# Optimization experiments

Hardware: AMD Instinct MI355X
Metric: run time of the kernel (lower is better)

## Reference

```python
import jax, jax.numpy as jnp
import numpy as np
from jax import lax


def setup_inputs() -> dict:
    key = jax.random.key(0)
    k1, k2 = jax.random.split(key)
    B, L1, L2, D = 128, 512, 512, 16
    s1_batch = jax.random.normal(k1, (B, L1, D), dtype=jnp.float32)
    s2_batch = jax.random.normal(k2, (B, L2, D), dtype=jnp.float32)
    return {"s1_batch": s1_batch, "s2_batch": s2_batch}


def _pairwise_sq_dists(s1, s2):
    # C[b,i,j] = sum_d (s1[b,i,d] - s2[b,j,d])^2, computed without a [B,L1,L2,D] temp
    s1sq = jnp.sum(s1 * s1, axis=-1)  # [B, L1]
    s2sq = jnp.sum(s2 * s2, axis=-1)  # [B, L2]
    cross = jnp.einsum("bid,bjd->bij", s1, s2)  # [B, L1, L2]
    return s1sq[:, :, None] + s2sq[:, None, :] - 2.0 * cross


def _dtw_final(C):
    # C: [B, L1, L2] cost matrix; returns DTW[:, -1, -1] via row-wise scan
    # Row 0: DTW[0, j] = cumsum of costs (only left moves allowed)
    row0 = jnp.cumsum(C[:, 0, :], axis=1)  # [B, L2]

    def row_step(prev_row, c_row):
        # prev_row, c_row: [B, L2]
        first = c_row[:, 0] + prev_row[:, 0]  # j = 0: only 'up' predecessor
        cs = c_row[:, 1:].T      # [L2-1, B]
        ups = prev_row[:, 1:].T  # DTW[i-1, j]
        dgs = prev_row[:, :-1].T # DTW[i-1, j-1]

        def col_step(left, xs):
            c_j, up, dg = xs
            val = c_j + jnp.minimum(left, jnp.minimum(up, dg))
            return val, val

        _, rest = lax.scan(col_step, first, (cs, ups, dgs))  # rest: [L2-1, B]
        new_row = jnp.concatenate([first[:, None], rest.T], axis=1)
        return new_row, None

    final_row, _ = lax.scan(row_step, row0, jnp.moveaxis(C[:, 1:, :], 1, 0))
    return final_row[:, -1]  # [B]


def reference(s1_batch, s2_batch):
    C = _pairwise_sq_dists(s1_batch, s2_batch)
    dtw_end = _dtw_final(C)
    return jnp.mean(jnp.sqrt(dtw_end))
```

## Files before the change

kernel.cpp:

```cpp
#include <hip/hip_runtime.h>
#include <math.h>


#define TL 512
#define TD 16
#define TNB 128
#define BIGF 3.0e38f
#define INFF __builtin_inff()
#define WOFF 71
#define EP 8
#define NE 99

typedef float f32x2 __attribute__((ext_vector_type(2)));
typedef float f32x4 __attribute__((ext_vector_type(4)));

__device__ inline f32x2 pk_fma(f32x2 a, f32x2 b, f32x2 c) {
    f32x2 d;
    asm("v_pk_fma_f32 %0, %1, %2, %3" : "=v"(d) : "v"(a), "v"(b), "v"(c));
    return d;
}
__device__ inline f32x2 pk_mul(f32x2 a, f32x2 b) {
    f32x2 d;
    asm("v_pk_mul_f32 %0, %1, %2" : "=v"(d) : "v"(a), "v"(b));
    return d;
}
__device__ inline float min3f(float a, float b, float c) {
    float d;
    asm("v_min3_f32 %0, %1, %2, %3" : "=v"(d) : "v"(a), "v"(b), "v"(c));
    return d;
}
template<int CTRL, int RM, bool BC>
__device__ inline float dpp_mov(float old_, float src) {
    return __int_as_float(__builtin_amdgcn_update_dpp(
        __float_as_int(old_), __float_as_int(src), CTRL, RM, 0xf, BC));
}

struct XR { f32x4 q0, q1, q2, q3; float sq; };

__device__ inline void xissue(unsigned xb, unsigned sb, int r, XR& x) {
    int rc = r < 0 ? 0 : (r > TL - 1 ? TL - 1 : r);
    unsigned a16 = xb + ((unsigned)rc << 4);
    unsigned a4  = sb + ((unsigned)rc << 2);
    asm volatile("ds_read_b128 %0, %1 offset:0"     : "=v"(x.q0) : "v"(a16));
    asm volatile("ds_read_b128 %0, %1 offset:8192"  : "=v"(x.q1) : "v"(a16));
    asm volatile("ds_read_b128 %0, %1 offset:16384" : "=v"(x.q2) : "v"(a16));
    asm volatile("ds_read_b128 %0, %1 offset:24576" : "=v"(x.q3) : "v"(a16));
    asm volatile("ds_read_b32  %0, %1 offset:0"     : "=v"(x.sq) : "v"(a4));
}

#define WAITC() { asm volatile("s_waitcnt lgkmcnt(10)" ::: "memory"); \
                  __builtin_amdgcn_sched_barrier(0); }

__device__ inline void sub(const XR& x, int r,
                           const f32x2 (&y0)[8], const f32x2 (&y1)[8],
                           f32x2 ys0, f32x2 ys1,
                           float& pv0, float& pv1, float& o1,
                           float bL, float bD, bool lane0) {
    const f32x2* xd = (const f32x2*)&x;
    f32x2 a0 = ys0, a1 = ys1;
    #pragma unroll
    for (int k = 0; k < 8; ++k) {
        a0 = pk_fma(xd[k], y0[k], a0);
        a1 = pk_fma(xd[k], y1[k], a1);
    }
    const float c0 = x.sq + (a0.x + a0.y);
    const float c1 = x.sq + (a1.x + a1.y);

    float left = dpp_mov<0x138, 0xf, false>(BIGF, pv1);
    float diag = dpp_mov<0x138, 0xf, false>(BIGF, o1);
    if (lane0) { left = bL; diag = bD; }
    o1 = pv1;

    const float v0 = c0 + min3f(pv0, left, diag);
    const float v1 = c1 + min3f(pv1, v0, pv0);
    const bool valid = (unsigned)r < (unsigned)TL;
    pv0 = valid ? v0 : pv0;
    pv1 = valid ? v1 : pv1;
}

__global__ __launch_bounds__(256, 1) void dtw_split_kernel(const float* __restrict__ s1,
                                                           const float* __restrict__ s2,
                                                           float* __restrict__ ws) {
    const int b   = blockIdx.x;
    const int tid = threadIdx.x;
    const int W   = tid >> 6;
    const int l   = tid & 63;

    __shared__ f32x4 xT[4][TL];
    __shared__ float sqT[TL];
    __shared__ f32x4 pkt[2][4][2];

    const float* s1b = s1 + (size_t)b * TL * TD;

    #pragma unroll
    for (int q = 0; q < 2; ++q) {
        const int r = 2 * tid + q;
        const f32x4* src = (const f32x4*)(s1b + r * TD);
        f32x4 q0 = src[0], q1 = src[1], q2 = src[2], q3 = src[3];
        xT[0][r] = q0; xT[1][r] = q1; xT[2][r] = q2; xT[3][r] = q3;
        f32x2 a_ = pk_mul(f32x2{q0.x, q0.y}, f32x2{q0.x, q0.y});
        a_ = pk_fma(f32x2{q0.z, q0.w}, f32x2{q0.z, q0.w}, a_);
        a_ = pk_fma(f32x2{q1.x, q1.y}, f32x2{q1.x, q1.y}, a_);
        a_ = pk_fma(f32x2{q1.z, q1.w}, f32x2{q1.z, q1.w}, a_);
        a_ = pk_fma(f32x2{q2.x, q2.y}, f32x2{q2.x, q2.y}, a_);
        a_ = pk_fma(f32x2{q2.z, q2.w}, f32x2{q2.z, q2.w}, a_);
        a_ = pk_fma(f32x2{q3.x, q3.y}, f32x2{q3.x, q3.y}, a_);
        a_ = pk_fma(f32x2{q3.z, q3.w}, f32x2{q3.z, q3.w}, a_);
        sqT[r] = a_.x + a_.y;
    }
    if (tid < 64) ((float*)pkt)[tid] = BIGF;

    const int j0 = 2 * (64 * W + l);
    f32x2 y0[8], y1[8];
    const float* yp0 = s2 + ((size_t)b * TL + j0) * TD;
    #pragma unroll
    for (int k = 0; k < 8; ++k) {
        y0[k] = *(const f32x2*)(yp0 + 2 * k);
        y1[k] = *(const f32x2*)(yp0 + TD + 2 * k);
    }
    f32x2 s0a = pk_mul(y0[0], y0[0]), s1a = pk_mul(y1[0], y1[0]);
    #pragma unroll
    for (int k = 1; k < 8; ++k) {
        s0a = pk_fma(y0[k], y0[k], s0a);
        s1a = pk_fma(y1[k], y1[k], s1a);
    }
    const f32x2 ys0 = {s0a.x + s0a.y, 0.f};
    const f32x2 ys1 = {s1a.x + s1a.y, 0.f};
    #pragma unroll
    for (int k = 0; k < 8; ++k) {
        y0[k] = pk_mul(y0[k], f32x2{-2.f, -2.f});
        y1[k] = pk_mul(y1[k], f32x2{-2.f, -2.f});
    }

    __syncthreads();

    const unsigned xb = (unsigned)(uintptr_t)&xT[0][0];
    const unsigned sb = (unsigned)(uintptr_t)&sqT[0];
    const int gL = WOFF * W + l;
    const bool lane0 = (l == 0);
    float pv0 = INFF, pv1 = INFF, o1 = INFF;
    float carry = (W == 0) ? 0.f : BIGF;

    XR x0, x1, x2, x3;
    xissue(xb, sb, 0 - gL, x0);
    xissue(xb, sb, 1 - gL, x1);
    xissue(xb, sb, 2 - gL, x2);

    for (int e = 0; e < NE; ++e) {
        float lb0 = BIGF, lb1 = BIGF, lb2 = BIGF, lb3 = BIGF;
        float lb4 = BIGF, lb5 = BIGF, lb6 = BIGF, lb7 = BIGF;
        if (W > 0) {
            f32x4 pA = pkt[(e + 1) & 1][W - 1][0];
            f32x4 pB = pkt[(e + 1) & 1][W - 1][1];
            lb0 = pA.x; lb1 = pA.y; lb2 = pA.z; lb3 = pA.w;
            lb4 = pB.x; lb5 = pB.y; lb6 = pB.z; lb7 = pB.w;
        }
        const int rb = EP * e - gL;
        float t0, t1, t2, t3, t4, t5, t6, t7;

        WAITC(); xissue(xb, sb, rb + 3,  x3);
        sub(x0, rb + 0, y0, y1, ys0, ys1, pv0, pv1, o1, lb0, carry, lane0); t0 = pv1;
        WAITC(); xissue(xb, sb, rb + 4,  x0);
        sub(x1, rb + 1, y0, y1, ys0, ys1, pv0, pv1, o1, lb1, lb0, lane0);   t1 = pv1;
        WAITC(); xissue(xb, sb, rb + 5,  x1);
        sub(x2, rb + 2, y0, y1, ys0, ys1, pv0, pv1, o1, lb2, lb1, lane0);   t2 = pv1;
        WAITC(); xissue(xb, sb, rb + 6,  x2);
        sub(x3, rb + 3, y0, y1, ys0, ys1, pv0, pv1, o1, lb3, lb2, lane0);   t3 = pv1;
        WAITC(); xissue(xb, sb, rb + 7,  x3);
        sub(x0, rb + 4, y0, y1, ys0, ys1, pv0, pv1, o1, lb4, lb3, lane0);   t4 = pv1;
        WAITC(); xissue(xb, sb, rb + 8,  x0);
        sub(x1, rb + 5, y0, y1, ys0, ys1, pv0, pv1, o1, lb5, lb4, lane0);   t5 = pv1;
        WAITC(); xissue(xb, sb, rb + 9,  x1);
        sub(x2, rb + 6, y0, y1, ys0, ys1, pv0, pv1, o1, lb6, lb5, lane0);   t6 = pv1;
        WAITC(); xissue(xb, sb, rb + 10, x2);
        sub(x3, rb + 7, y0, y1, ys0, ys1, pv0, pv1, o1, lb7, lb6, lane0);   t7 = pv1;

        carry = lb7;

        if (l == 63 && W < 3) {
            pkt[e & 1][W][0] = f32x4{t0, t1, t2, t3};
            pkt[e & 1][W][1] = f32x4{t4, t5, t6, t7};
        }
        __syncthreads();
    }

    if (W == 3 && l == 63) ws[b] = sqrtf(pv1);
}

__global__ void dtw_reduce_kernel(const float* __restrict__ ws, float* __restrict__ out) {
    const int t = threadIdx.x;
    float v = ws[t] + ws[t + 64];
    #pragma unroll
    for (int d2 = 32; d2 > 0; d2 >>= 1) v += __shfl_down(v, d2);
    if (t == 0) out[0] = v * (1.0f / TNB);
}

extern "C" void kernel_launch(void* const* d_in, const int* in_sizes, int n_in,
                              void* d_out, int out_size, void* d_ws, size_t ws_size,
                              hipStream_t stream) {
    const float* s1 = (const float*)d_in[0];
    const float* s2 = (const float*)d_in[1];
    float* ws  = (float*)d_ws;
    float* out = (float*)d_out;

    dtw_split_kernel<<<TNB, 256, 0, stream>>>(s1, s2, ws);
    dtw_reduce_kernel<<<1, 64, 0, stream>>>(ws, out);
}
```

Before: 95.95 us.

## Assign four DTW columns per thread and run the wavefront with two waves

Each thread now owns four adjacent columns of the DTW matrix instead of two, so a block uses two wavefronts (128 threads) instead of four. The anti-diagonal pipeline shortens from 99 to 81 epochs, and fewer inter-wave handoffs and barriers are needed. In exchange, each step does twice the packed-FMA work and has a longer serial min-add chain per thread. Only half as many SIMDs per CU are used.

```diff
diff --git a/kernel.cpp b/kernel.cpp
--- a/kernel.cpp
+++ b/kernel.cpp
@@ -9,7 +9,7 @@
 #define INFF __builtin_inff()
 #define WOFF 71
 #define EP 8
-#define NE 99
+#define NE 81
 
 typedef float f32x2 __attribute__((ext_vector_type(2)));
 typedef float f32x4 __attribute__((ext_vector_type(4)));
@@ -53,32 +53,41 @@
 
 __device__ inline void sub(const XR& x, int r,
                            const f32x2 (&y0)[8], const f32x2 (&y1)[8],
-                           f32x2 ys0, f32x2 ys1,
-                           float& pv0, float& pv1, float& o1,
-                           float bL, float bD, bool lane0) {
+                           const f32x2 (&y2)[8], const f32x2 (&y3)[8],
+                           f32x2 ys0, f32x2 ys1, f32x2 ys2, f32x2 ys3,
+                           float& pv0, float& pv1, float& pv2, float& pv3,
+                           float& o3, float bL, float bD, bool lane0) {
     const f32x2* xd = (const f32x2*)&x;
-    f32x2 a0 = ys0, a1 = ys1;
+    f32x2 a0 = ys0, a1 = ys1, a2 = ys2, a3 = ys3;
     #pragma unroll
     for (int k = 0; k < 8; ++k) {
         a0 = pk_fma(xd[k], y0[k], a0);
         a1 = pk_fma(xd[k], y1[k], a1);
+        a2 = pk_fma(xd[k], y2[k], a2);
+        a3 = pk_fma(xd[k], y3[k], a3);
     }
     const float c0 = x.sq + (a0.x + a0.y);
     const float c1 = x.sq + (a1.x + a1.y);
-
-    float left = dpp_mov<0x138, 0xf, false>(BIGF, pv1);
-    float diag = dpp_mov<0x138, 0xf, false>(BIGF, o1);
+    const float c2 = x.sq + (a2.x + a2.y);
+    const float c3 = x.sq + (a3.x + a3.y);
+
+    float left = dpp_mov<0x138, 0xf, false>(BIGF, pv3);
+    float diag = dpp_mov<0x138, 0xf, false>(BIGF, o3);
     if (lane0) { left = bL; diag = bD; }
-    o1 = pv1;
+    o3 = pv3;
 
     const float v0 = c0 + min3f(pv0, left, diag);
     const float v1 = c1 + min3f(pv1, v0, pv0);
+    const float v2 = c2 + min3f(pv2, v1, pv1);
+    const float v3 = c3 + min3f(pv3, v2, pv2);
     const bool valid = (unsigned)r < (unsigned)TL;
     pv0 = valid ? v0 : pv0;
     pv1 = valid ? v1 : pv1;
-}
-
-__global__ __launch_bounds__(256, 1) void dtw_split_kernel(const float* __restrict__ s1,
+    pv2 = valid ? v2 : pv2;
+    pv3 = valid ? v3 : pv3;
+}
+
+__global__ __launch_bounds__(128, 1) void dtw_split_kernel(const float* __restrict__ s1,
                                                            const float* __restrict__ s2,
                                                            float* __restrict__ ws) {
     const int b   = blockIdx.x;
@@ -88,13 +97,13 @@
 
     __shared__ f32x4 xT[4][TL];
     __shared__ float sqT[TL];
-    __shared__ f32x4 pkt[2][4][2];
+    __shared__ f32x4 pkt[2][2];
 
     const float* s1b = s1 + (size_t)b * TL * TD;
 
     #pragma unroll
-    for (int q = 0; q < 2; ++q) {
-        const int r = 2 * tid + q;
+    for (int q = 0; q < 4; ++q) {
+        const int r = tid + 128 * q;
         const f32x4* src = (const f32x4*)(s1b + r * TD);
         f32x4 q0 = src[0], q1 = src[1], q2 = src[2], q3 = src[3];
         xT[0][r] = q0; xT[1][r] = q1; xT[2][r] = q2; xT[3][r] = q3;
@@ -108,28 +117,37 @@
         a_ = pk_fma(f32x2{q3.z, q3.w}, f32x2{q3.z, q3.w}, a_);
         sqT[r] = a_.x + a_.y;
     }
-    if (tid < 64) ((float*)pkt)[tid] = BIGF;
-
-    const int j0 = 2 * (64 * W + l);
-    f32x2 y0[8], y1[8];
-    const float* yp0 = s2 + ((size_t)b * TL + j0) * TD;
+    if (tid < 16) ((float*)pkt)[tid] = BIGF;
+
+    const int j0 = 4 * (64 * W + l);
+    const float* yp = s2 + ((size_t)b * TL + j0) * TD;
+    f32x2 y0[8], y1[8], y2[8], y3[8];
     #pragma unroll
     for (int k = 0; k < 8; ++k) {
-        y0[k] = *(const f32x2*)(yp0 + 2 * k);
-        y1[k] = *(const f32x2*)(yp0 + TD + 2 * k);
+        y0[k] = *(const volatile f32x2*)(yp + 0 * TD + 2 * k);
+        y1[k] = *(const volatile f32x2*)(yp + 1 * TD + 2 * k);
+        y2[k] = *(const volatile f32x2*)(yp + 2 * TD + 2 * k);
+        y3[k] = *(const volatile f32x2*)(yp + 3 * TD + 2 * k);
     }
     f32x2 s0a = pk_mul(y0[0], y0[0]), s1a = pk_mul(y1[0], y1[0]);
+    f32x2 s2a = pk_mul(y2[0], y2[0]), s3a = pk_mul(y3[0], y3[0]);
     #pragma unroll
     for (int k = 1; k < 8; ++k) {
         s0a = pk_fma(y0[k], y0[k], s0a);
         s1a = pk_fma(y1[k], y1[k], s1a);
+        s2a = pk_fma(y2[k], y2[k], s2a);
+        s3a = pk_fma(y3[k], y3[k], s3a);
     }
     const f32x2 ys0 = {s0a.x + s0a.y, 0.f};
     const f32x2 ys1 = {s1a.x + s1a.y, 0.f};
+    const f32x2 ys2 = {s2a.x + s2a.y, 0.f};
+    const f32x2 ys3 = {s3a.x + s3a.y, 0.f};
     #pragma unroll
     for (int k = 0; k < 8; ++k) {
         y0[k] = pk_mul(y0[k], f32x2{-2.f, -2.f});
         y1[k] = pk_mul(y1[k], f32x2{-2.f, -2.f});
+        y2[k] = pk_mul(y2[k], f32x2{-2.f, -2.f});
+        y3[k] = pk_mul(y3[k], f32x2{-2.f, -2.f});
     }
 
     __syncthreads();
@@ -138,7 +156,7 @@
     const unsigned sb = (unsigned)(uintptr_t)&sqT[0];
     const int gL = WOFF * W + l;
     const bool lane0 = (l == 0);
-    float pv0 = INFF, pv1 = INFF, o1 = INFF;
+    float pv0 = INFF, pv1 = INFF, pv2 = INFF, pv3 = INFF, o3 = INFF;
     float carry = (W == 0) ? 0.f : BIGF;
 
     XR x0, x1, x2, x3;
@@ -150,8 +168,8 @@
         float lb0 = BIGF, lb1 = BIGF, lb2 = BIGF, lb3 = BIGF;
         float lb4 = BIGF, lb5 = BIGF, lb6 = BIGF, lb7 = BIGF;
         if (W > 0) {
-            f32x4 pA = pkt[(e + 1) & 1][W - 1][0];
-            f32x4 pB = pkt[(e + 1) & 1][W - 1][1];
+            f32x4 pA = pkt[(e + 1) & 1][0];
+            f32x4 pB = pkt[(e + 1) & 1][1];
             lb0 = pA.x; lb1 = pA.y; lb2 = pA.z; lb3 = pA.w;
             lb4 = pB.x; lb5 = pB.y; lb6 = pB.z; lb7 = pB.w;
         }
@@ -159,32 +177,40 @@
         float t0, t1, t2, t3, t4, t5, t6, t7;
 
         WAITC(); xissue(xb, sb, rb + 3,  x3);
-        sub(x0, rb + 0, y0, y1, ys0, ys1, pv0, pv1, o1, lb0, carry, lane0); t0 = pv1;
+        sub(x0, rb + 0, y0, y1, y2, y3, ys0, ys1, ys2, ys3,
+            pv0, pv1, pv2, pv3, o3, lb0, carry, lane0); t0 = pv3;
         WAITC(); xissue(xb, sb, rb + 4,  x0);
-        sub(x1, rb + 1, y0, y1, ys0, ys1, pv0, pv1, o1, lb1, lb0, lane0);   t1 = pv1;
+        sub(x1, rb + 1, y0, y1, y2, y3, ys0, ys1, ys2, ys3,
+            pv0, pv1, pv2, pv3, o3, lb1, lb0, lane0);   t1 = pv3;
         WAITC(); xissue(xb, sb, rb + 5,  x1);
-        sub(x2, rb + 2, y0, y1, ys0, ys1, pv0, pv1, o1, lb2, lb1, lane0);   t2 = pv1;
+        sub(x2, rb + 2, y0, y1, y2, y3, ys0, ys1, ys2, ys3,
+            pv0, pv1, pv2, pv3, o3, lb2, lb1, lane0);   t2 = pv3;
         WAITC(); xissue(xb, sb, rb + 6,  x2);
-        sub(x3, rb + 3, y0, y1, ys0, ys1, pv0, pv1, o1, lb3, lb2, lane0);   t3 = pv1;
+        sub(x3, rb + 3, y0, y1, y2, y3, ys0, ys1, ys2, ys3,
+            pv0, pv1, pv2, pv3, o3, lb3, lb2, lane0);   t3 = pv3;
         WAITC(); xissue(xb, sb, rb + 7,  x3);
-        sub(x0, rb + 4, y0, y1, ys0, ys1, pv0, pv1, o1, lb4, lb3, lane0);   t4 = pv1;
+        sub(x0, rb + 4, y0, y1, y2, y3, ys0, ys1, ys2, ys3,
+            pv0, pv1, pv2, pv3, o3, lb4, lb3, lane0);   t4 = pv3;
         WAITC(); xissue(xb, sb, rb + 8,  x0);
-        sub(x1, rb + 5, y0, y1, ys0, ys1, pv0, pv1, o1, lb5, lb4, lane0);   t5 = pv1;
+        sub(x1, rb + 5, y0, y1, y2, y3, ys0, ys1, ys2, ys3,
+            pv0, pv1, pv2, pv3, o3, lb5, lb4, lane0);   t5 = pv3;
         WAITC(); xissue(xb, sb, rb + 9,  x1);
-        sub(x2, rb + 6, y0, y1, ys0, ys1, pv0, pv1, o1, lb6, lb5, lane0);   t6 = pv1;
+        sub(x2, rb + 6, y0, y1, y2, y3, ys0, ys1, ys2, ys3,
+            pv0, pv1, pv2, pv3, o3, lb6, lb5, lane0);   t6 = pv3;
         WAITC(); xissue(xb, sb, rb + 10, x2);
-        sub(x3, rb + 7, y0, y1, ys0, ys1, pv0, pv1, o1, lb7, lb6, lane0);   t7 = pv1;
+        sub(x3, rb + 7, y0, y1, y2, y3, ys0, ys1, ys2, ys3,
+            pv0, pv1, pv2, pv3, o3, lb7, lb6, lane0);   t7 = pv3;
 
         carry = lb7;
 
-        if (l == 63 && W < 3) {
-            pkt[e & 1][W][0] = f32x4{t0, t1, t2, t3};
-            pkt[e & 1][W][1] = f32x4{t4, t5, t6, t7};
+        if (l == 63 && W == 0) {
+            pkt[e & 1][0] = f32x4{t0, t1, t2, t3};
+            pkt[e & 1][1] = f32x4{t4, t5, t6, t7};
         }
         __syncthreads();
     }
 
-    if (W == 3 && l == 63) ws[b] = sqrtf(pv1);
+    if (W == 1 && l == 63) ws[b] = sqrtf(pv3);
 }
 
 __global__ void dtw_reduce_kernel(const float* __restrict__ ws, float* __restrict__ out) {
@@ -203,6 +229,6 @@
     float* ws  = (float*)d_ws;
     float* out = (float*)d_out;
 
-    dtw_split_kernel<<<TNB, 256, 0, stream>>>(s1, s2, ws);
+    dtw_split_kernel<<<TNB, 128, 0, stream>>>(s1, s2, ws);
     dtw_reduce_kernel<<<1, 64, 0, stream>>>(ws, out);
 }
```

After: 113.6 us. 1.18x slower.
